# Optimization experiments

Measured on AMD Instinct MI355X. Metric: run time of the kernel, lower is better.

Reference implementation:

```python
import jax, jax.numpy as jnp
import numpy as np

B, S, C, H, D = 4, 2048, 512, 8, 64
EPS = 1e-5
SCALE = D ** -0.5


def layer_norm(x, w, b):
    m = jnp.mean(x, axis=-1, keepdims=True)
    v = jnp.var(x, axis=-1, keepdims=True)
    return (x - m) * jax.lax.rsqrt(v + EPS) * w + b


def setup_inputs() -> dict:
    key = jax.random.key(0)
    ks = jax.random.split(key, 7)
    s = 0.02
    return {
        "x": jax.random.normal(ks[0], (B, S, C), jnp.float32),
        "Wq": jax.random.normal(ks[1], (C, H * D), jnp.float32) * s,
        "Wk": jax.random.normal(ks[2], (C, H * D), jnp.float32) * s,
        "Wv": jax.random.normal(ks[3], (C, H * D), jnp.float32) * s,
        "Wo": jax.random.normal(ks[4], (H * D, C), jnp.float32) * s,
        "ln1_w": jnp.ones((C,), jnp.float32), "ln1_b": jnp.zeros((C,), jnp.float32),
        "ff_ln1_w": jnp.ones((C,), jnp.float32), "ff_ln1_b": jnp.zeros((C,), jnp.float32),
        "ff_w1": jax.random.normal(ks[5], (C, C), jnp.float32) * s, "ff_b1": jnp.zeros((C,), jnp.float32),
        "ff_ln2_w": jnp.ones((C,), jnp.float32), "ff_ln2_b": jnp.zeros((C,), jnp.float32),
        "ff_w2": jax.random.normal(ks[6], (C, C), jnp.float32) * s, "ff_b2": jnp.zeros((C,), jnp.float32),
        "ln2_w": jnp.ones((C,), jnp.float32), "ln2_b": jnp.zeros((C,), jnp.float32),
    }


def causal_attention(x, Wq, Wk, Wv, Wo):
    # Mathematically identical to the bucketed memory-efficient attention:
    # online-softmax bucketing changes compute order, not the result.
    q = (x @ Wq).reshape(B, S, H, D).transpose(0, 2, 1, 3)  # [B,H,S,D]
    k = (x @ Wk).reshape(B, S, H, D).transpose(0, 2, 1, 3)
    v = (x @ Wv).reshape(B, S, H, D).transpose(0, 2, 1, 3)
    scores = jnp.einsum('bhqd,bhkd->bhqk', q, k) * SCALE  # [B,H,S,S]
    causal = jnp.tril(jnp.ones((S, S), bool))
    scores = jnp.where(causal, scores, jnp.finfo(scores.dtype).min)
    attn = jax.nn.softmax(scores, axis=-1)
    out = jnp.einsum('bhqk,bhkd->bhqd', attn, v)
    out = out.transpose(0, 2, 1, 3).reshape(B, S, H * D)
    return out @ Wo


def reference(x, Wq, Wk, Wv, Wo, ln1_w, ln1_b, ff_ln1_w, ff_ln1_b, ff_w1, ff_b1,
              ff_ln2_w, ff_ln2_b, ff_w2, ff_b2, ln2_w, ln2_b):
    a = causal_attention(x, Wq, Wk, Wv, Wo)
    x_ln = layer_norm(a + x, ln1_w, ln1_b)
    h = layer_norm(x_ln, ff_ln1_w, ff_ln1_b) @ ff_w1 + ff_b1
    h = layer_norm(h, ff_ln2_w, ff_ln2_b) @ ff_w2 + ff_b2
    return layer_norm(h + x_ln, ln2_w, ln2_b)
```

## Files before the change

kernel.cpp:

```cpp
#include <hip/hip_runtime.h>

#define B_ 4
#define S_ 2048
#define C_ 512
#define H_ 8
#define D_ 64
#define M_ 8192

typedef short s8v __attribute__((ext_vector_type(8)));
typedef short s4v __attribute__((ext_vector_type(4)));
typedef float f4v __attribute__((ext_vector_type(4)));
typedef unsigned short u16;
typedef unsigned int u32;

__device__ __forceinline__ u16 f2b(float f) {
    u32 u = __builtin_bit_cast(u32, f);
    u = u + 0x7fffu + ((u >> 16) & 1u);
    return (u16)(u >> 16);
}

__device__ __forceinline__ void b2f8(const s8v v, float* f) {
    #pragma unroll
    for (int k = 0; k < 8; ++k)
        f[k] = __builtin_bit_cast(float, (u32)(u16)v[k] << 16);
}

__device__ __forceinline__ void gl2lds16(const void* g, void* l) {
    __builtin_amdgcn_global_load_lds(
        (const __attribute__((address_space(1))) void*)g,
        (__attribute__((address_space(3))) void*)l, 16, 0, 0);
}

__global__ __launch_bounds__(256) void prep_k(const float* __restrict__ x,
                                              u16* __restrict__ xb,
                                              const float* __restrict__ s0,
                                              const float* __restrict__ s1,
                                              const float* __restrict__ s2,
                                              const float* __restrict__ s3,
                                              const float* __restrict__ s4,
                                              const float* __restrict__ s5,
                                              u16* __restrict__ d0,
                                              u16* __restrict__ d1,
                                              u16* __restrict__ d2,
                                              u16* __restrict__ d3,
                                              u16* __restrict__ d4,
                                              u16* __restrict__ d5)
{
    __shared__ float t[32][33];
    const int bx = blockIdx.x;
    if (bx < 4096) {
        const int i = (bx * 256 + (int)threadIdx.x) * 4;
        const float4 v = *(const float4*)&x[i];
        ushort4 o;
        o.x = f2b(v.x); o.y = f2b(v.y); o.z = f2b(v.z); o.w = f2b(v.w);
        *(ushort4*)&xb[i] = o;
        return;
    }
    const int tb = bx - 4096;
    const int z = tb >> 8, rem = tb & 255;
    const float* W; u16* Wt;
    switch (z) {
        case 0: W = s0; Wt = d0; break;
        case 1: W = s1; Wt = d1; break;
        case 2: W = s2; Wt = d2; break;
        case 3: W = s3; Wt = d3; break;
        case 4: W = s4; Wt = d4; break;
        default: W = s5; Wt = d5; break;
    }
    const int tx = threadIdx.x & 31, ty = threadIdx.x >> 5;
    const int n0 = (rem & 15) * 32, k0 = (rem >> 4) * 32;
    #pragma unroll
    for (int i = 0; i < 4; ++i)
        t[ty + i * 8][tx] = W[(size_t)(k0 + ty + i * 8) * C_ + n0 + tx];
    __syncthreads();
    #pragma unroll
    for (int i = 0; i < 4; ++i)
        Wt[(size_t)(n0 + ty + i * 8) * C_ + k0 + tx] = f2b(t[tx][ty + i * 8]);
}

template <bool OB>
__global__ __launch_bounds__(256) void gemm_k(const u16* __restrict__ A,
                                              const u16* __restrict__ Bt,
                                              const float* __restrict__ bias,
                                              void* __restrict__ outv)
{
    __shared__ u16 As[2][128][64];
    __shared__ u16 Bs[2][64][64];
    const int tid = threadIdx.x;
    const int lane = tid & 63, w = tid >> 6;
    const int q4 = lane >> 4, l16 = lane & 15;
    const int wr = w >> 1, wc = w & 1;
    const int bm = blockIdx.x * 128, bn = blockIdx.y * 64;
    const int sr8  = lane >> 3;
    const int scol = ((lane & 7) ^ sr8) * 8;

    f4v acc[4][2];
    #pragma unroll
    for (int i = 0; i < 4; ++i)
        #pragma unroll
        for (int j = 0; j < 2; ++j) acc[i][j] = (f4v){0.f, 0.f, 0.f, 0.f};

    const u16* Ab = A  + (size_t)bm * C_;
    const u16* Bb = Bt + (size_t)bn * C_;

    auto stage = [&](int bf, int kt) {
        const int k0 = kt * 64;
        #pragma unroll
        for (int t = 0; t < 4; ++t)
            gl2lds16(Ab + (size_t)(w * 32 + t * 8 + sr8) * C_ + k0 + scol,
                     (char*)As + bf * 16384 + (w * 32 + t * 8) * 128);
        #pragma unroll
        for (int t = 0; t < 2; ++t)
            gl2lds16(Bb + (size_t)(w * 16 + t * 8 + sr8) * C_ + k0 + scol,
                     (char*)Bs + bf * 8192 + (w * 16 + t * 8) * 128);
    };

    stage(0, 0);
    for (int kt = 0; kt < 8; ++kt) {
        __syncthreads();
        const int bf = kt & 1;
        if (kt < 7) stage(bf ^ 1, kt + 1);
        #pragma unroll
        for (int kk = 0; kk < 2; ++kk) {
            const int pc = ((kk * 4 + q4) ^ (l16 & 7)) * 8;
            s8v a[4], b[2];
            #pragma unroll
            for (int i = 0; i < 4; ++i)
                a[i] = *(const s8v*)&As[bf][wr * 64 + i * 16 + l16][pc];
            #pragma unroll
            for (int j = 0; j < 2; ++j)
                b[j] = *(const s8v*)&Bs[bf][wc * 32 + j * 16 + l16][pc];
            #pragma unroll
            for (int i = 0; i < 4; ++i)
                #pragma unroll
                for (int j = 0; j < 2; ++j)
                    acc[i][j] = __builtin_amdgcn_mfma_f32_16x16x32_bf16(a[i], b[j], acc[i][j], 0, 0, 0);
        }
    }

    #pragma unroll
    for (int j = 0; j < 2; ++j) {
        const int n = bn + wc * 32 + j * 16 + l16;
        const float bj = bias ? bias[n] : 0.0f;
        #pragma unroll
        for (int i = 0; i < 4; ++i) {
            const int m = bm + wr * 64 + i * 16 + q4 * 4;
            #pragma unroll
            for (int reg = 0; reg < 4; ++reg) {
                const float vv = acc[i][j][reg] + bj;
                if constexpr (OB) ((u16*)outv)[(size_t)(m + reg) * C_ + n] = f2b(vv);
                else              ((float*)outv)[(size_t)(m + reg) * C_ + n] = vv;
            }
        }
    }
}

__global__ __launch_bounds__(256) void qkv_k(const u16* __restrict__ A,
                                             const u16* __restrict__ Wq,
                                             const u16* __restrict__ Wk,
                                             const u16* __restrict__ Wv,
                                             u16* __restrict__ oq,
                                             u16* __restrict__ ok,
                                             u16* __restrict__ ovt)
{
    __shared__ u16 As[2][128][64];
    __shared__ u16 Bs[2][64][64];
    const int tid = threadIdx.x;
    const int lane = tid & 63, w = tid >> 6;
    const int q4 = lane >> 4, l16 = lane & 15;
    const int wr = w >> 1, wc = w & 1;
    const int nt = blockIdx.y, which = nt >> 3;
    const u16* Bt = which == 0 ? Wq : (which == 1 ? Wk : Wv);
    const int bm = blockIdx.x * 128, bn = (nt & 7) * 64;
    const int sr8  = lane >> 3;
    const int scol = ((lane & 7) ^ sr8) * 8;

    f4v acc[4][2];
    #pragma unroll
    for (int i = 0; i < 4; ++i)
        #pragma unroll
        for (int j = 0; j < 2; ++j) acc[i][j] = (f4v){0.f, 0.f, 0.f, 0.f};

    const u16* Ab = A  + (size_t)bm * C_;
    const u16* Bb = Bt + (size_t)bn * C_;

    auto stage = [&](int bf, int kt) {
        const int k0 = kt * 64;
        #pragma unroll
        for (int t = 0; t < 4; ++t)
            gl2lds16(Ab + (size_t)(w * 32 + t * 8 + sr8) * C_ + k0 + scol,
                     (char*)As + bf * 16384 + (w * 32 + t * 8) * 128);
        #pragma unroll
        for (int t = 0; t < 2; ++t)
            gl2lds16(Bb + (size_t)(w * 16 + t * 8 + sr8) * C_ + k0 + scol,
                     (char*)Bs + bf * 8192 + (w * 16 + t * 8) * 128);
    };

    stage(0, 0);
    for (int kt = 0; kt < 8; ++kt) {
        __syncthreads();
        const int bf = kt & 1;
        if (kt < 7) stage(bf ^ 1, kt + 1);
        #pragma unroll
        for (int kk = 0; kk < 2; ++kk) {
            const int pc = ((kk * 4 + q4) ^ (l16 & 7)) * 8;
            s8v a[4], b[2];
            #pragma unroll
            for (int i = 0; i < 4; ++i)
                a[i] = *(const s8v*)&As[bf][wr * 64 + i * 16 + l16][pc];
            #pragma unroll
            for (int j = 0; j < 2; ++j)
                b[j] = *(const s8v*)&Bs[bf][wc * 32 + j * 16 + l16][pc];
            #pragma unroll
            for (int i = 0; i < 4; ++i)
                #pragma unroll
                for (int j = 0; j < 2; ++j)
                    acc[i][j] = __builtin_amdgcn_mfma_f32_16x16x32_bf16(a[i], b[j], acc[i][j], 0, 0, 0);
        }
    }

    if (which == 0) {
        #pragma unroll
        for (int j = 0; j < 2; ++j) {
            const int n = bn + wc * 32 + j * 16 + l16;
            #pragma unroll
            for (int i = 0; i < 4; ++i) {
                const int m = bm + wr * 64 + i * 16 + q4 * 4;
                #pragma unroll
                for (int reg = 0; reg < 4; ++reg)
                    oq[(size_t)(m + reg) * C_ + n] = f2b(acc[i][j][reg]);
            }
        }
    } else if (which == 1) {
        #pragma unroll
        for (int j = 0; j < 2; ++j) {
            const int n = bn + wc * 32 + j * 16 + l16;
            const int nswz = (n & ~31) | ((((n >> 3) & 3) ^ q4) << 3) | (n & 7);
            #pragma unroll
            for (int i = 0; i < 4; ++i) {
                const int m = bm + wr * 64 + i * 16 + q4 * 4;
                #pragma unroll
                for (int reg = 0; reg < 4; ++reg)
                    ok[(size_t)(m + reg) * C_ + nswz] = f2b(acc[i][j][reg]);
            }
        }
    } else {
        const int bglob = bm >> 11;
        const int sbase = bm & (S_ - 1);
        #pragma unroll
        for (int j = 0; j < 2; ++j) {
            const int n = bn + wc * 32 + j * 16 + l16;
            const int h = n >> 6, d = n & 63;
            u16* vrow = ovt + ((size_t)(bglob * H_ + h) * D_ + d) * S_;
            const int xw = d & 7;
            #pragma unroll
            for (int i = 0; i < 4; ++i) {
                const int s = sbase + wr * 64 + i * 16 + q4 * 4;
                const int pg = ((s & 31) >> 2) ^ xw;
                s4v pv;
                #pragma unroll
                for (int reg = 0; reg < 4; ++reg) pv[reg] = (short)f2b(acc[i][j][reg]);
                *(s4v*)&vrow[(s & ~31) + (pg << 2)] = pv;
            }
        }
    }
}

__global__ __launch_bounds__(256) void ln2xb_k(const u16* __restrict__ in,
                                               const float* __restrict__ res,
                                               const float* __restrict__ w1,
                                               const float* __restrict__ b1,
                                               const float* __restrict__ w2,
                                               const float* __restrict__ b2,
                                               u16* __restrict__ out1,
                                               u16* __restrict__ out2)
{
    const int lane = threadIdx.x & 63;
    const int row  = blockIdx.x * 4 + (threadIdx.x >> 6);
    const size_t off = (size_t)row * C_ + lane * 8;
    float v[8];
    b2f8(*(const s8v*)&in[off], v);
    {
        const float4 r0 = *(const float4*)&res[off];
        const float4 r1 = *(const float4*)&res[off + 4];
        v[0] += r0.x; v[1] += r0.y; v[2] += r0.z; v[3] += r0.w;
        v[4] += r1.x; v[5] += r1.y; v[6] += r1.z; v[7] += r1.w;
    }
    float s = 0.f, ss = 0.f;
    #pragma unroll
    for (int k = 0; k < 8; ++k) { s += v[k]; ss += v[k] * v[k]; }
    #pragma unroll
    for (int o = 32; o >= 1; o >>= 1) { s += __shfl_xor(s, o); ss += __shfl_xor(ss, o); }
    float mean = s * (1.0f / C_);
    float rstd = rsqrtf(ss * (1.0f / C_) - mean * mean + 1e-5f);

    const float4 wA0 = *(const float4*)&w1[lane * 8];
    const float4 wA1 = *(const float4*)&w1[lane * 8 + 4];
    const float4 bA0 = *(const float4*)&b1[lane * 8];
    const float4 bA1 = *(const float4*)&b1[lane * 8 + 4];
    const float wA[8] = {wA0.x, wA0.y, wA0.z, wA0.w, wA1.x, wA1.y, wA1.z, wA1.w};
    const float bA[8] = {bA0.x, bA0.y, bA0.z, bA0.w, bA1.x, bA1.y, bA1.z, bA1.w};
    float y[8];
    s8v o1;
    #pragma unroll
    for (int k = 0; k < 8; ++k) {
        y[k] = (v[k] - mean) * rstd * wA[k] + bA[k];
        o1[k] = (short)f2b(y[k]);
    }
    *(s8v*)&out1[off] = o1;

    s = 0.f; ss = 0.f;
    #pragma unroll
    for (int k = 0; k < 8; ++k) { s += y[k]; ss += y[k] * y[k]; }
    #pragma unroll
    for (int o = 32; o >= 1; o >>= 1) { s += __shfl_xor(s, o); ss += __shfl_xor(ss, o); }
    mean = s * (1.0f / C_);
    rstd = rsqrtf(ss * (1.0f / C_) - mean * mean + 1e-5f);

    const float4 wB0 = *(const float4*)&w2[lane * 8];
    const float4 wB1 = *(const float4*)&w2[lane * 8 + 4];
    const float4 bB0 = *(const float4*)&b2[lane * 8];
    const float4 bB1 = *(const float4*)&b2[lane * 8 + 4];
    const float wB[8] = {wB0.x, wB0.y, wB0.z, wB0.w, wB1.x, wB1.y, wB1.z, wB1.w};
    const float bB[8] = {bB0.x, bB0.y, bB0.z, bB0.w, bB1.x, bB1.y, bB1.z, bB1.w};
    s8v o2;
    #pragma unroll
    for (int k = 0; k < 8; ++k)
        o2[k] = (short)f2b((y[k] - mean) * rstd * wB[k] + bB[k]);
    *(s8v*)&out2[off] = o2;
}

__global__ __launch_bounds__(256) void lnb_k(const u16* __restrict__ in,
                                             const float* __restrict__ w,
                                             const float* __restrict__ bb,
                                             u16* __restrict__ out)
{
    const int lane = threadIdx.x & 63;
    const int row  = blockIdx.x * 4 + (threadIdx.x >> 6);
    const size_t off = (size_t)row * C_ + lane * 8;
    float v[8];
    b2f8(*(const s8v*)&in[off], v);
    float s = 0.f, ss = 0.f;
    #pragma unroll
    for (int k = 0; k < 8; ++k) { s += v[k]; ss += v[k] * v[k]; }
    #pragma unroll
    for (int o = 32; o >= 1; o >>= 1) { s += __shfl_xor(s, o); ss += __shfl_xor(ss, o); }
    const float mean = s * (1.0f / C_);
    const float rstd = rsqrtf(ss * (1.0f / C_) - mean * mean + 1e-5f);
    const float4 w0 = *(const float4*)&w[lane * 8];
    const float4 w1 = *(const float4*)&w[lane * 8 + 4];
    const float4 b0 = *(const float4*)&bb[lane * 8];
    const float4 b1 = *(const float4*)&bb[lane * 8 + 4];
    const float wv[8] = {w0.x, w0.y, w0.z, w0.w, w1.x, w1.y, w1.z, w1.w};
    const float bv[8] = {b0.x, b0.y, b0.z, b0.w, b1.x, b1.y, b1.z, b1.w};
    s8v o;
    #pragma unroll
    for (int k = 0; k < 8; ++k)
        o[k] = (short)f2b((v[k] - mean) * rstd * wv[k] + bv[k]);
    *(s8v*)&out[off] = o;
}

__global__ __launch_bounds__(256) void lnfin_k(const u16* __restrict__ in,
                                               const u16* __restrict__ res,
                                               const float* __restrict__ w,
                                               const float* __restrict__ bb,
                                               float* __restrict__ out)
{
    const int lane = threadIdx.x & 63;
    const int row  = blockIdx.x * 4 + (threadIdx.x >> 6);
    const size_t off = (size_t)row * C_ + lane * 8;
    float v[8], r[8];
    b2f8(*(const s8v*)&in[off], v);
    b2f8(*(const s8v*)&res[off], r);
    #pragma unroll
    for (int k = 0; k < 8; ++k) v[k] += r[k];
    float s = 0.f, ss = 0.f;
    #pragma unroll
    for (int k = 0; k < 8; ++k) { s += v[k]; ss += v[k] * v[k]; }
    #pragma unroll
    for (int o = 32; o >= 1; o >>= 1) { s += __shfl_xor(s, o); ss += __shfl_xor(ss, o); }
    const float mean = s * (1.0f / C_);
    const float rstd = rsqrtf(ss * (1.0f / C_) - mean * mean + 1e-5f);
    const float4 w0 = *(const float4*)&w[lane * 8];
    const float4 w1 = *(const float4*)&w[lane * 8 + 4];
    const float4 b0 = *(const float4*)&bb[lane * 8];
    const float4 b1 = *(const float4*)&bb[lane * 8 + 4];
    const float wv[8] = {w0.x, w0.y, w0.z, w0.w, w1.x, w1.y, w1.z, w1.w};
    const float bv[8] = {b0.x, b0.y, b0.z, b0.w, b1.x, b1.y, b1.z, b1.w};
    float4 o0, o1;
    o0.x = (v[0] - mean) * rstd * wv[0] + bv[0];
    o0.y = (v[1] - mean) * rstd * wv[1] + bv[1];
    o0.z = (v[2] - mean) * rstd * wv[2] + bv[2];
    o0.w = (v[3] - mean) * rstd * wv[3] + bv[3];
    o1.x = (v[4] - mean) * rstd * wv[4] + bv[4];
    o1.y = (v[5] - mean) * rstd * wv[5] + bv[5];
    o1.z = (v[6] - mean) * rstd * wv[6] + bv[6];
    o1.w = (v[7] - mean) * rstd * wv[7] + bv[7];
    *(float4*)&out[off]     = o0;
    *(float4*)&out[off + 4] = o1;
}

__global__ __launch_bounds__(256) void attn_k(const u16* __restrict__ Q,
                                              const u16* __restrict__ K,
                                              const u16* __restrict__ Vt,
                                              u16* __restrict__ O)
{
    __shared__ u16 Ks[2][2][64][32];
    __shared__ u16 Vs[2][2][64][32];
    const int tid = threadIdx.x;
    const int lane = tid & 63, w = tid >> 6;
    const int q4 = lane >> 4, l16 = lane & 15;
    const int h = blockIdx.y, b = blockIdx.z;
    const int qb = 31 - (int)blockIdx.x;
    const size_t base  = ((size_t)b * S_) * C_ + h * D_;
    const size_t basev = ((size_t)(b * H_ + h)) * D_ * S_;
    const int lr = lane >> 2, lc = (lane & 3) * 8;
    const int kq = (q4 ^ ((l16 >> 2) & 3)) * 8;

    s8v qf[2];
    #pragma unroll
    for (int kh = 0; kh < 2; ++kh)
        qf[kh] = *(const s8v*)&Q[base + (size_t)(qb * 64 + w * 16 + l16) * C_ + kh * 32 + q4 * 8];

    #pragma unroll
    for (int r = 0; r < 2; ++r) {
        const int seg = r * 4 + w;
        const int row = (seg & 3) * 16 + lr;
        const int kh = seg >> 2;
        gl2lds16(K  + base  + (size_t)row * C_ + kh * 32 + lc, (char*)Ks + seg * 1024);
        gl2lds16(Vt + basev + (size_t)row * S_ + kh * 32 + lc, (char*)Vs + seg * 1024);
    }

    f4v o[4];
    float lp[4] = {0.f, 0.f, 0.f, 0.f};
    #pragma unroll
    for (int j = 0; j < 4; ++j) o[j] = (f4v){0.f, 0.f, 0.f, 0.f};

    const int qrow = w * 16 + l16;
    for (int kb = 0; kb <= qb; ++kb) {
        __syncthreads();
        const int buf = kb & 1;
        if (kb < qb) {
            const int nb = buf ^ 1, kn = kb + 1;
            #pragma unroll
            for (int r = 0; r < 2; ++r) {
                const int seg = r * 4 + w;
                const int row = (seg & 3) * 16 + lr;
                const int kh = seg >> 2;
                gl2lds16(K  + base  + (size_t)(kn * 64 + row) * C_ + kh * 32 + lc,
                         (char*)Ks + nb * 8192 + seg * 1024);
                gl2lds16(Vt + basev + (size_t)row * S_ + kn * 64 + kh * 32 + lc,
                         (char*)Vs + nb * 8192 + seg * 1024);
            }
        }

        f4v sc[4];
        #pragma unroll
        for (int j = 0; j < 4; ++j) sc[j] = (f4v){0.f, 0.f, 0.f, 0.f};
        #pragma unroll
        for (int kh = 0; kh < 2; ++kh) {
            #pragma unroll
            for (int j = 0; j < 4; ++j) {
                const s8v kf = *(const s8v*)&Ks[buf][kh][j * 16 + l16][kq];
                sc[j] = __builtin_amdgcn_mfma_f32_16x16x32_bf16(kf, qf[kh], sc[j], 0, 0, 0);
            }
        }

        s4v pa[4];
        if (kb == qb) {
            #pragma unroll
            for (int j = 0; j < 4; ++j) {
                float ps = 0.0f;
                #pragma unroll
                for (int reg = 0; reg < 4; ++reg) {
                    float t = fmaf(sc[j][reg], 0.18033688011112043f, -11.541560327111707f);
                    if ((j * 16 + q4 * 4 + reg) > qrow) t = -128.0f;
                    const float p = exp2f(t);
                    ps += p;
                    pa[j][reg] = (short)(__builtin_bit_cast(u32, p) >> 16);
                }
                lp[j] += ps;
            }
        } else {
            #pragma unroll
            for (int j = 0; j < 4; ++j) {
                float ps = 0.0f;
                #pragma unroll
                for (int reg = 0; reg < 4; ++reg) {
                    const float p = exp2f(fmaf(sc[j][reg], 0.18033688011112043f,
                                               -11.541560327111707f));
                    ps += p;
                    pa[j][reg] = (short)(__builtin_bit_cast(u32, p) >> 16);
                }
                lp[j] += ps;
            }
        }

        #pragma unroll
        for (int c = 0; c < 4; ++c) {
            const int gh = (((c & 1) * 4 + q4) ^ (l16 & 7)) * 4;
            #pragma unroll
            for (int dj = 0; dj < 4; ++dj) {
                const s4v vb = *(const s4v*)&Vs[buf][c >> 1][dj * 16 + l16][gh];
                o[dj] = __builtin_amdgcn_mfma_f32_16x16x16bf16_1k(pa[c], vb, o[dj], 0, 0, 0);
            }
        }
    }

    float lt = (lp[0] + lp[1]) + (lp[2] + lp[3]);
    lt += __shfl_xor(lt, 16);
    lt += __shfl_xor(lt, 32);
    #pragma unroll
    for (int reg = 0; reg < 4; ++reg) {
        const float inv = 1.0f / __shfl(lt, q4 * 4 + reg);
        const size_t rowoff = base + (size_t)(qb * 64 + w * 16 + q4 * 4 + reg) * C_;
        #pragma unroll
        for (int dj = 0; dj < 4; ++dj)
            O[rowoff + dj * 16 + l16] = f2b(o[dj][reg] * inv);
    }
}

extern "C" void kernel_launch(void* const* d_in, const int* in_sizes, int n_in,
                              void* d_out, int out_size, void* d_ws, size_t ws_size,
                              hipStream_t stream)
{
    const float* x       = (const float*)d_in[0];
    const float* Wq      = (const float*)d_in[1];
    const float* Wk      = (const float*)d_in[2];
    const float* Wv      = (const float*)d_in[3];
    const float* Wo      = (const float*)d_in[4];
    const float* ln1_w   = (const float*)d_in[5];
    const float* ln1_b   = (const float*)d_in[6];
    const float* ffln1_w = (const float*)d_in[7];
    const float* ffln1_b = (const float*)d_in[8];
    const float* ff_w1   = (const float*)d_in[9];
    const float* ff_b1   = (const float*)d_in[10];
    const float* ffln2_w = (const float*)d_in[11];
    const float* ffln2_b = (const float*)d_in[12];
    const float* ff_w2   = (const float*)d_in[13];
    const float* ff_b2   = (const float*)d_in[14];
    const float* ln2_w   = (const float*)d_in[15];
    const float* ln2_b   = (const float*)d_in[16];
    float* out = (float*)d_out;

    const size_t MC = (size_t)M_ * C_;
    const size_t WW = (size_t)C_ * C_;
    u16* xb   = (u16*)d_ws;
    u16* WqT  = xb + MC;
    u16* WkT  = WqT + WW;
    u16* WvT  = WkT + WW;
    u16* WoT  = WvT + WW;
    u16* W1T  = WoT + WW;
    u16* W2T  = W1T + WW;
    u16* qbuf = W2T + WW;
    u16* kbuf = qbuf + MC;
    u16* vbuf = kbuf + MC;
    u16* vtbuf= vbuf + MC;
    u16*  abuf = xb;
    u16*  tf   = qbuf;
    u16*  xln  = vbuf;

    const dim3 gg(M_ / 128, C_ / 64);
    const dim3 gq(M_ / 128, 24);
    const dim3 ga(32, H_, B_);
    const int  gl = M_ / 4;

    prep_k<<<5632, 256, 0, stream>>>(x, xb, Wq, Wk, Wv, Wo, ff_w1, ff_w2,
                                     WqT, WkT, WvT, WoT, W1T, W2T);

    qkv_k<<<gq, 256, 0, stream>>>(xb, WqT, WkT, WvT, qbuf, kbuf, vtbuf);
    attn_k<<<ga, 256, 0, stream>>>(qbuf, kbuf, vtbuf, abuf);

    gemm_k<true><<<gg, 256, 0, stream>>>(abuf, WoT, nullptr, tf);
    ln2xb_k<<<gl, 256, 0, stream>>>(tf, x, ln1_w, ln1_b, ffln1_w, ffln1_b,
                                    xln, xb);
    gemm_k<true><<<gg, 256, 0, stream>>>(xb, W1T, ff_b1, tf);
    lnb_k<<<gl, 256, 0, stream>>>(tf, ffln2_w, ffln2_b, xb);
    gemm_k<true><<<gg, 256, 0, stream>>>(xb, W2T, ff_b2, tf);
    lnfin_k<<<gl, 256, 0, stream>>>(tf, xln, ln2_w, ln2_b, out);
}
```

Baseline: 242.7 us.

## Pair causal query blocks per workgroup and raise MFMA wave priority

Each attention workgroup now handles two query blocks, qb and 31-qb, so every workgroup does the same amount of causal work. The grid halves to 16 blocks in x. The first K/V tile for the second block is prefetched while the first block's output is written. s_setprio is raised around the MFMA sections so matrix work gets issue priority over other waves. The cost is half as many workgroups (512), which lowers parallelism and occupancy slack. Each workgroup also runs sequentially for longer.

```diff
diff --git a/kernel.cpp b/kernel.cpp
--- a/kernel.cpp
+++ b/kernel.cpp
@@ -411,113 +411,136 @@
     const int lane = tid & 63, w = tid >> 6;
     const int q4 = lane >> 4, l16 = lane & 15;
     const int h = blockIdx.y, b = blockIdx.z;
-    const int qb = 31 - (int)blockIdx.x;
     const size_t base  = ((size_t)b * S_) * C_ + h * D_;
     const size_t basev = ((size_t)(b * H_ + h)) * D_ * S_;
     const int lr = lane >> 2, lc = (lane & 3) * 8;
     const int kq = (q4 ^ ((l16 >> 2) & 3)) * 8;
-
+    const int qrow = w * 16 + l16;
+
+    const u16* kbase = K  + base  + (size_t)(w * 16 + lr) * C_ + lc;
+    const u16* vbase = Vt + basev + (size_t)(w * 16 + lr) * S_ + lc;
+    char* kd0 = (char*)Ks + w * 1024;
+    char* kd1 = (char*)Ks + (4 + w) * 1024;
+    char* vd0 = (char*)Vs + w * 1024;
+    char* vd1 = (char*)Vs + (4 + w) * 1024;
+
+    f4v o[4];
+    float lp[4];
     s8v qf[2];
-    #pragma unroll
-    for (int kh = 0; kh < 2; ++kh)
-        qf[kh] = *(const s8v*)&Q[base + (size_t)(qb * 64 + w * 16 + l16) * C_ + kh * 32 + q4 * 8];
-
-    #pragma unroll
-    for (int r = 0; r < 2; ++r) {
-        const int seg = r * 4 + w;
-        const int row = (seg & 3) * 16 + lr;
-        const int kh = seg >> 2;
-        gl2lds16(K  + base  + (size_t)row * C_ + kh * 32 + lc, (char*)Ks + seg * 1024);
-        gl2lds16(Vt + basev + (size_t)row * S_ + kh * 32 + lc, (char*)Vs + seg * 1024);
-    }
-
-    f4v o[4];
-    float lp[4] = {0.f, 0.f, 0.f, 0.f};
-    #pragma unroll
-    for (int j = 0; j < 4; ++j) o[j] = (f4v){0.f, 0.f, 0.f, 0.f};
-
-    const int qrow = w * 16 + l16;
-    for (int kb = 0; kb <= qb; ++kb) {
-        __syncthreads();
-        const int buf = kb & 1;
-        if (kb < qb) {
-            const int nb = buf ^ 1, kn = kb + 1;
-            #pragma unroll
-            for (int r = 0; r < 2; ++r) {
-                const int seg = r * 4 + w;
-                const int row = (seg & 3) * 16 + lr;
-                const int kh = seg >> 2;
-                gl2lds16(K  + base  + (size_t)(kn * 64 + row) * C_ + kh * 32 + lc,
-                         (char*)Ks + nb * 8192 + seg * 1024);
-                gl2lds16(Vt + basev + (size_t)row * S_ + kn * 64 + kh * 32 + lc,
-                         (char*)Vs + nb * 8192 + seg * 1024);
-            }
-        }
-
-        f4v sc[4];
-        #pragma unroll
-        for (int j = 0; j < 4; ++j) sc[j] = (f4v){0.f, 0.f, 0.f, 0.f};
-        #pragma unroll
-        for (int kh = 0; kh < 2; ++kh) {
-            #pragma unroll
-            for (int j = 0; j < 4; ++j) {
-                const s8v kf = *(const s8v*)&Ks[buf][kh][j * 16 + l16][kq];
-                sc[j] = __builtin_amdgcn_mfma_f32_16x16x32_bf16(kf, qf[kh], sc[j], 0, 0, 0);
-            }
-        }
-
-        s4v pa[4];
-        if (kb == qb) {
-            #pragma unroll
-            for (int j = 0; j < 4; ++j) {
-                float ps = 0.0f;
-                #pragma unroll
-                for (int reg = 0; reg < 4; ++reg) {
-                    float t = fmaf(sc[j][reg], 0.18033688011112043f, -11.541560327111707f);
-                    if ((j * 16 + q4 * 4 + reg) > qrow) t = -128.0f;
-                    const float p = exp2f(t);
-                    ps += p;
-                    pa[j][reg] = (short)(__builtin_bit_cast(u32, p) >> 16);
+
+    auto stage0 = [&]() {
+        gl2lds16(kbase,      kd0);
+        gl2lds16(kbase + 32, kd1);
+        gl2lds16(vbase,      vd0);
+        gl2lds16(vbase + 32, vd1);
+    };
+    auto loadq = [&](int qb) {
+        #pragma unroll
+        for (int kh = 0; kh < 2; ++kh)
+            qf[kh] = *(const s8v*)&Q[base + (size_t)(qb * 64 + qrow) * C_ + kh * 32 + q4 * 8];
+        #pragma unroll
+        for (int j = 0; j < 4; ++j) { o[j] = (f4v){0.f, 0.f, 0.f, 0.f}; lp[j] = 0.f; }
+    };
+
+    auto kbloop = [&](int qb) {
+        const u16* kp = kbase + 64 * C_;
+        const u16* vp = vbase + 64;
+        for (int kb = 0; kb <= qb; ++kb) {
+            __syncthreads();
+            const int buf = kb & 1;
+            if (kb < qb) {
+                const int nb = (buf ^ 1) * 8192;
+                gl2lds16(kp,      kd0 + nb);
+                gl2lds16(kp + 32, kd1 + nb);
+                gl2lds16(vp,      vd0 + nb);
+                gl2lds16(vp + 32, vd1 + nb);
+                kp += 64 * C_;
+                vp += 64;
+            }
+
+            f4v sc[4];
+            #pragma unroll
+            for (int j = 0; j < 4; ++j) sc[j] = (f4v){0.f, 0.f, 0.f, 0.f};
+            __builtin_amdgcn_s_setprio(1);
+            #pragma unroll
+            for (int kh = 0; kh < 2; ++kh) {
+                #pragma unroll
+                for (int j = 0; j < 4; ++j) {
+                    const s8v kf = *(const s8v*)&Ks[buf][kh][j * 16 + l16][kq];
+                    sc[j] = __builtin_amdgcn_mfma_f32_16x16x32_bf16(kf, qf[kh], sc[j], 0, 0, 0);
                 }
-                lp[j] += ps;
-            }
-        } else {
-            #pragma unroll
-            for (int j = 0; j < 4; ++j) {
-                float ps = 0.0f;
-                #pragma unroll
-                for (int reg = 0; reg < 4; ++reg) {
-                    const float p = exp2f(fmaf(sc[j][reg], 0.18033688011112043f,
-                                               -11.541560327111707f));
-                    ps += p;
-                    pa[j][reg] = (short)(__builtin_bit_cast(u32, p) >> 16);
+            }
+            __builtin_amdgcn_s_setprio(0);
+
+            s4v pa[4];
+            if (kb == qb) {
+                #pragma unroll
+                for (int j = 0; j < 4; ++j) {
+                    float ps = 0.0f;
+                    #pragma unroll
+                    for (int reg = 0; reg < 4; ++reg) {
+                        float t = fmaf(sc[j][reg], 0.18033688011112043f, -11.541560327111707f);
+                        if ((j * 16 + q4 * 4 + reg) > qrow) t = -128.0f;
+                        const float p = exp2f(t);
+                        ps += p;
+                        pa[j][reg] = (short)(__builtin_bit_cast(u32, p) >> 16);
+                    }
+                    lp[j] += ps;
                 }
-                lp[j] += ps;
-            }
-        }
-
-        #pragma unroll
-        for (int c = 0; c < 4; ++c) {
-            const int gh = (((c & 1) * 4 + q4) ^ (l16 & 7)) * 4;
-            #pragma unroll
-            for (int dj = 0; dj < 4; ++dj) {
-                const s4v vb = *(const s4v*)&Vs[buf][c >> 1][dj * 16 + l16][gh];
-                o[dj] = __builtin_amdgcn_mfma_f32_16x16x16bf16_1k(pa[c], vb, o[dj], 0, 0, 0);
-            }
-        }
-    }
-
-    float lt = (lp[0] + lp[1]) + (lp[2] + lp[3]);
-    lt += __shfl_xor(lt, 16);
-    lt += __shfl_xor(lt, 32);
-    #pragma unroll
-    for (int reg = 0; reg < 4; ++reg) {
-        const float inv = 1.0f / __shfl(lt, q4 * 4 + reg);
-        const size_t rowoff = base + (size_t)(qb * 64 + w * 16 + q4 * 4 + reg) * C_;
-        #pragma unroll
-        for (int dj = 0; dj < 4; ++dj)
-            O[rowoff + dj * 16 + l16] = f2b(o[dj][reg] * inv);
-    }
+            } else {
+                #pragma unroll
+                for (int j = 0; j < 4; ++j) {
+                    float ps = 0.0f;
+                    #pragma unroll
+                    for (int reg = 0; reg < 4; ++reg) {
+                        const float p = exp2f(fmaf(sc[j][reg], 0.18033688011112043f,
+                                                   -11.541560327111707f));
+                        ps += p;
+                        pa[j][reg] = (short)(__builtin_bit_cast(u32, p) >> 16);
+                    }
+                    lp[j] += ps;
+                }
+            }
+
+            __builtin_amdgcn_s_setprio(1);
+            #pragma unroll
+            for (int c = 0; c < 4; ++c) {
+                const int gh = (((c & 1) * 4 + q4) ^ (l16 & 7)) * 4;
+                #pragma unroll
+                for (int dj = 0; dj < 4; ++dj) {
+                    const s4v vb = *(const s4v*)&Vs[buf][c >> 1][dj * 16 + l16][gh];
+                    o[dj] = __builtin_amdgcn_mfma_f32_16x16x16bf16_1k(pa[c], vb, o[dj], 0, 0, 0);
+                }
+            }
+            __builtin_amdgcn_s_setprio(0);
+        }
+    };
+
+    auto writeout = [&](int qb) {
+        float lt = (lp[0] + lp[1]) + (lp[2] + lp[3]);
+        lt += __shfl_xor(lt, 16);
+        lt += __shfl_xor(lt, 32);
+        #pragma unroll
+        for (int reg = 0; reg < 4; ++reg) {
+            const float inv = 1.0f / __shfl(lt, q4 * 4 + reg);
+            const size_t rowoff = base + (size_t)(qb * 64 + w * 16 + q4 * 4 + reg) * C_;
+            #pragma unroll
+            for (int dj = 0; dj < 4; ++dj)
+                O[rowoff + dj * 16 + l16] = f2b(o[dj][reg] * inv);
+        }
+    };
+
+    int qb = 31 - (int)blockIdx.x;
+    stage0();
+    loadq(qb);
+    kbloop(qb);
+    __syncthreads();
+    stage0();
+    writeout(qb);
+    const int qb1 = (int)blockIdx.x;
+    loadq(qb1);
+    kbloop(qb1);
+    writeout(qb1);
 }
 
 extern "C" void kernel_launch(void* const* d_in, const int* in_sizes, int n_in,
@@ -562,7 +585,7 @@
 
     const dim3 gg(M_ / 128, C_ / 64);
     const dim3 gq(M_ / 128, 24);
-    const dim3 ga(32, H_, B_);
+    const dim3 ga(16, H_, B_);
     const int  gl = M_ / 4;
 
     prep_k<<<5632, 256, 0, stream>>>(x, xb, Wq, Wk, Wv, Wo, ff_w1, ff_w2,
```

Measured after the change: 228.5 us. -5.9%, faster.

## Pair causal query blocks per workgroup and split KV steps across two wave groups

Applied to the files above, without the earlier changes.

The attention kernel now processes a heavy and a light query block (qH=31-px, qL=px) in one 512-thread workgroup, so every block does exactly 33 KV tiles and the causal work is balanced. Two groups of four waves take alternating KV steps through a 4-slot LDS ring, then merge their partial accumulators and row sums through shared memory before normalising. It also raises MFMA sections with s_setprio. The grid is halved, and LDS use grows to 64KB per block, which may limit occupancy and adds a reduction step.

```diff
diff --git a/kernel.cpp b/kernel.cpp
--- a/kernel.cpp
+++ b/kernel.cpp
@@ -400,123 +400,209 @@
     *(float4*)&out[off + 4] = o1;
 }
 
-__global__ __launch_bounds__(256) void attn_k(const u16* __restrict__ Q,
-                                              const u16* __restrict__ K,
-                                              const u16* __restrict__ Vt,
-                                              u16* __restrict__ O)
-{
-    __shared__ u16 Ks[2][2][64][32];
-    __shared__ u16 Vs[2][2][64][32];
+__global__ __launch_bounds__(512, 4) void attn_k(const u16* __restrict__ Q,
+                                                 const u16* __restrict__ K,
+                                                 const u16* __restrict__ Vt,
+                                                 u16* __restrict__ O)
+{
+    __shared__ char smem[65536];
+    u16* KsB = (u16*)smem;
+    u16* VsB = (u16*)(smem + 32768);
     const int tid = threadIdx.x;
     const int lane = tid & 63, w = tid >> 6;
+    const int grp = w >> 2, wl = w & 3;
     const int q4 = lane >> 4, l16 = lane & 15;
     const int h = blockIdx.y, b = blockIdx.z;
-    const int qb = 31 - (int)blockIdx.x;
+    const int px = blockIdx.x;
+    const int qH = 31 - px, qL = px;
+    const int nH = 32 - px;
     const size_t base  = ((size_t)b * S_) * C_ + h * D_;
     const size_t basev = ((size_t)(b * H_ + h)) * D_ * S_;
     const int lr = lane >> 2, lc = (lane & 3) * 8;
     const int kq = (q4 ^ ((l16 >> 2) & 3)) * 8;
+    const int qrow = wl * 16 + l16;
+
+    auto stage = [&](int kb, int sl) {
+        #pragma unroll
+        for (int r = 0; r < 2; ++r) {
+            const int seg = r * 4 + wl;
+            const int row = (seg & 3) * 16 + lr;
+            const int kh = seg >> 2;
+            gl2lds16(K  + base  + (size_t)(kb * 64 + row) * C_ + kh * 32 + lc,
+                     (char*)KsB + sl * 8192 + seg * 1024);
+            gl2lds16(Vt + basev + (size_t)row * S_ + kb * 64 + kh * 32 + lc,
+                     (char*)VsB + sl * 8192 + seg * 1024);
+        }
+    };
 
     s8v qf[2];
     #pragma unroll
     for (int kh = 0; kh < 2; ++kh)
-        qf[kh] = *(const s8v*)&Q[base + (size_t)(qb * 64 + w * 16 + l16) * C_ + kh * 32 + q4 * 8];
-
-    #pragma unroll
-    for (int r = 0; r < 2; ++r) {
-        const int seg = r * 4 + w;
-        const int row = (seg & 3) * 16 + lr;
-        const int kh = seg >> 2;
-        gl2lds16(K  + base  + (size_t)row * C_ + kh * 32 + lc, (char*)Ks + seg * 1024);
-        gl2lds16(Vt + basev + (size_t)row * S_ + kh * 32 + lc, (char*)Vs + seg * 1024);
-    }
-
-    f4v o[4];
-    float lp[4] = {0.f, 0.f, 0.f, 0.f};
-    #pragma unroll
-    for (int j = 0; j < 4; ++j) o[j] = (f4v){0.f, 0.f, 0.f, 0.f};
-
-    const int qrow = w * 16 + l16;
-    for (int kb = 0; kb <= qb; ++kb) {
+        qf[kh] = *(const s8v*)&Q[base + (size_t)(qH * 64 + qrow) * C_ + kh * 32 + q4 * 8];
+
+    f4v acc[4]; float lp[4];
+    f4v oH[4];  float lpH[4];
+    #pragma unroll
+    for (int j = 0; j < 4; ++j) {
+        acc[j] = (f4v){0.f, 0.f, 0.f, 0.f}; lp[j] = 0.f;
+        oH[j]  = (f4v){0.f, 0.f, 0.f, 0.f}; lpH[j] = 0.f;
+    }
+    bool dumped = false;
+
+    stage(grp, grp);
+
+    for (int t = 0; t <= 16; ++t) {
         __syncthreads();
-        const int buf = kb & 1;
-        if (kb < qb) {
-            const int nb = buf ^ 1, kn = kb + 1;
-            #pragma unroll
-            for (int r = 0; r < 2; ++r) {
-                const int seg = r * 4 + w;
-                const int row = (seg & 3) * 16 + lr;
-                const int kh = seg >> 2;
-                gl2lds16(K  + base  + (size_t)(kn * 64 + row) * C_ + kh * 32 + lc,
-                         (char*)Ks + nb * 8192 + seg * 1024);
-                gl2lds16(Vt + basev + (size_t)row * S_ + kn * 64 + kh * 32 + lc,
-                         (char*)Vs + nb * 8192 + seg * 1024);
-            }
-        }
-
-        f4v sc[4];
-        #pragma unroll
-        for (int j = 0; j < 4; ++j) sc[j] = (f4v){0.f, 0.f, 0.f, 0.f};
-        #pragma unroll
-        for (int kh = 0; kh < 2; ++kh) {
-            #pragma unroll
-            for (int j = 0; j < 4; ++j) {
-                const s8v kf = *(const s8v*)&Ks[buf][kh][j * 16 + l16][kq];
-                sc[j] = __builtin_amdgcn_mfma_f32_16x16x32_bf16(kf, qf[kh], sc[j], 0, 0, 0);
-            }
-        }
-
-        s4v pa[4];
-        if (kb == qb) {
-            #pragma unroll
-            for (int j = 0; j < 4; ++j) {
-                float ps = 0.0f;
-                #pragma unroll
-                for (int reg = 0; reg < 4; ++reg) {
-                    float t = fmaf(sc[j][reg], 0.18033688011112043f, -11.541560327111707f);
-                    if ((j * 16 + q4 * 4 + reg) > qrow) t = -128.0f;
-                    const float p = exp2f(t);
-                    ps += p;
-                    pa[j][reg] = (short)(__builtin_bit_cast(u32, p) >> 16);
+        const int s = 2 * t + grp;
+        if (s <= 32) {
+            const int s2 = s + 2;
+            if (s2 <= 32) {
+                const int kb2 = s2 < nH ? s2 : s2 - nH;
+                stage(kb2, s2 & 3);
+            }
+            if (s >= nH && !dumped) {
+                dumped = true;
+                #pragma unroll
+                for (int j = 0; j < 4; ++j) {
+                    oH[j] = acc[j]; lpH[j] = lp[j];
+                    acc[j] = (f4v){0.f, 0.f, 0.f, 0.f}; lp[j] = 0.f;
                 }
-                lp[j] += ps;
-            }
+                #pragma unroll
+                for (int kh = 0; kh < 2; ++kh)
+                    qf[kh] = *(const s8v*)&Q[base + (size_t)(qL * 64 + qrow) * C_ + kh * 32 + q4 * 8];
+            }
+            const int kb = s < nH ? s : s - nH;
+            const int sl = s & 3;
+            const u16* ks = KsB + sl * 4096;
+            const u16* vs = VsB + sl * 4096;
+
+            f4v sc[4];
+            #pragma unroll
+            for (int j = 0; j < 4; ++j) sc[j] = (f4v){0.f, 0.f, 0.f, 0.f};
+            __builtin_amdgcn_s_setprio(1);
+            #pragma unroll
+            for (int kh = 0; kh < 2; ++kh) {
+                #pragma unroll
+                for (int j = 0; j < 4; ++j) {
+                    const s8v kf = *(const s8v*)&ks[(kh * 64 + j * 16 + l16) * 32 + kq];
+                    sc[j] = __builtin_amdgcn_mfma_f32_16x16x32_bf16(kf, qf[kh], sc[j], 0, 0, 0);
+                }
+            }
+            __builtin_amdgcn_s_setprio(0);
+
+            s4v pa[4];
+            const bool diag = (s == nH - 1) || (s == 32);
+            if (diag) {
+                #pragma unroll
+                for (int j = 0; j < 4; ++j) {
+                    float ps = 0.0f;
+                    #pragma unroll
+                    for (int reg = 0; reg < 4; ++reg) {
+                        float tt = fmaf(sc[j][reg], 0.18033688011112043f, -11.541560327111707f);
+                        if ((j * 16 + q4 * 4 + reg) > qrow) tt = -128.0f;
+                        const float p = exp2f(tt);
+                        ps += p;
+                        pa[j][reg] = (short)(__builtin_bit_cast(u32, p) >> 16);
+                    }
+                    lp[j] += ps;
+                }
+            } else {
+                #pragma unroll
+                for (int j = 0; j < 4; ++j) {
+                    float ps = 0.0f;
+                    #pragma unroll
+                    for (int reg = 0; reg < 4; ++reg) {
+                        const float p = exp2f(fmaf(sc[j][reg], 0.18033688011112043f,
+                                                   -11.541560327111707f));
+                        ps += p;
+                        pa[j][reg] = (short)(__builtin_bit_cast(u32, p) >> 16);
+                    }
+                    lp[j] += ps;
+                }
+            }
+
+            __builtin_amdgcn_s_setprio(1);
+            #pragma unroll
+            for (int c = 0; c < 4; ++c) {
+                const int gh = (((c & 1) * 4 + q4) ^ (l16 & 7)) * 4;
+                #pragma unroll
+                for (int dj = 0; dj < 4; ++dj) {
+                    const s4v vb = *(const s4v*)&vs[((c >> 1) * 64 + dj * 16 + l16) * 32 + gh];
+                    acc[dj] = __builtin_amdgcn_mfma_f32_16x16x16bf16_1k(pa[c], vb, acc[dj], 0, 0, 0);
+                }
+            }
+            __builtin_amdgcn_s_setprio(0);
+        }
+    }
+
+    if (!dumped) {
+        #pragma unroll
+        for (int j = 0; j < 4; ++j) {
+            oH[j] = acc[j]; lpH[j] = lp[j];
+            acc[j] = (f4v){0.f, 0.f, 0.f, 0.f}; lp[j] = 0.f;
+        }
+    }
+
+    __syncthreads();
+    float* exH = (float*)smem;
+    float* exL = (float*)(smem + 20480);
+    {
+        float* p = (grp ? exH : exL) + (wl * 64 + lane) * 20;
+        if (grp) {
+            #pragma unroll
+            for (int dj = 0; dj < 4; ++dj)
+                #pragma unroll
+                for (int reg = 0; reg < 4; ++reg) p[dj * 4 + reg] = oH[dj][reg];
+            #pragma unroll
+            for (int j = 0; j < 4; ++j) p[16 + j] = lpH[j];
         } else {
             #pragma unroll
-            for (int j = 0; j < 4; ++j) {
-                float ps = 0.0f;
-                #pragma unroll
-                for (int reg = 0; reg < 4; ++reg) {
-                    const float p = exp2f(fmaf(sc[j][reg], 0.18033688011112043f,
-                                               -11.541560327111707f));
-                    ps += p;
-                    pa[j][reg] = (short)(__builtin_bit_cast(u32, p) >> 16);
-                }
-                lp[j] += ps;
-            }
-        }
-
-        #pragma unroll
-        for (int c = 0; c < 4; ++c) {
-            const int gh = (((c & 1) * 4 + q4) ^ (l16 & 7)) * 4;
-            #pragma unroll
-            for (int dj = 0; dj < 4; ++dj) {
-                const s4v vb = *(const s4v*)&Vs[buf][c >> 1][dj * 16 + l16][gh];
-                o[dj] = __builtin_amdgcn_mfma_f32_16x16x16bf16_1k(pa[c], vb, o[dj], 0, 0, 0);
-            }
-        }
-    }
-
-    float lt = (lp[0] + lp[1]) + (lp[2] + lp[3]);
-    lt += __shfl_xor(lt, 16);
-    lt += __shfl_xor(lt, 32);
-    #pragma unroll
-    for (int reg = 0; reg < 4; ++reg) {
-        const float inv = 1.0f / __shfl(lt, q4 * 4 + reg);
-        const size_t rowoff = base + (size_t)(qb * 64 + w * 16 + q4 * 4 + reg) * C_;
+            for (int dj = 0; dj < 4; ++dj)
+                #pragma unroll
+                for (int reg = 0; reg < 4; ++reg) p[dj * 4 + reg] = acc[dj][reg];
+            #pragma unroll
+            for (int j = 0; j < 4; ++j) p[16 + j] = lp[j];
+        }
+    }
+    __syncthreads();
+    if (grp == 0) {
+        const float* p = exH + (wl * 64 + lane) * 20;
         #pragma unroll
         for (int dj = 0; dj < 4; ++dj)
-            O[rowoff + dj * 16 + l16] = f2b(o[dj][reg] * inv);
+            #pragma unroll
+            for (int reg = 0; reg < 4; ++reg) oH[dj][reg] += p[dj * 4 + reg];
+        #pragma unroll
+        for (int j = 0; j < 4; ++j) lpH[j] += p[16 + j];
+        float lt = (lpH[0] + lpH[1]) + (lpH[2] + lpH[3]);
+        lt += __shfl_xor(lt, 16);
+        lt += __shfl_xor(lt, 32);
+        #pragma unroll
+        for (int reg = 0; reg < 4; ++reg) {
+            const float inv = 1.0f / __shfl(lt, q4 * 4 + reg);
+            const size_t rowoff = base + (size_t)(qH * 64 + wl * 16 + q4 * 4 + reg) * C_;
+            #pragma unroll
+            for (int dj = 0; dj < 4; ++dj)
+                O[rowoff + dj * 16 + l16] = f2b(oH[dj][reg] * inv);
+        }
+    } else {
+        const float* p = exL + (wl * 64 + lane) * 20;
+        #pragma unroll
+        for (int dj = 0; dj < 4; ++dj)
+            #pragma unroll
+            for (int reg = 0; reg < 4; ++reg) acc[dj][reg] += p[dj * 4 + reg];
+        #pragma unroll
+        for (int j = 0; j < 4; ++j) lp[j] += p[16 + j];
+        float lt = (lp[0] + lp[1]) + (lp[2] + lp[3]);
+        lt += __shfl_xor(lt, 16);
+        lt += __shfl_xor(lt, 32);
+        #pragma unroll
+        for (int reg = 0; reg < 4; ++reg) {
+            const float inv = 1.0f / __shfl(lt, q4 * 4 + reg);
+            const size_t rowoff = base + (size_t)(qL * 64 + wl * 16 + q4 * 4 + reg) * C_;
+            #pragma unroll
+            for (int dj = 0; dj < 4; ++dj)
+                O[rowoff + dj * 16 + l16] = f2b(acc[dj][reg] * inv);
+        }
     }
 }
 
@@ -562,14 +648,14 @@
 
     const dim3 gg(M_ / 128, C_ / 64);
     const dim3 gq(M_ / 128, 24);
-    const dim3 ga(32, H_, B_);
+    const dim3 ga(16, H_, B_);
     const int  gl = M_ / 4;
 
     prep_k<<<5632, 256, 0, stream>>>(x, xb, Wq, Wk, Wv, Wo, ff_w1, ff_w2,
                                      WqT, WkT, WvT, WoT, W1T, W2T);
 
     qkv_k<<<gq, 256, 0, stream>>>(xb, WqT, WkT, WvT, qbuf, kbuf, vtbuf);
-    attn_k<<<ga, 256, 0, stream>>>(qbuf, kbuf, vtbuf, abuf);
+    attn_k<<<ga, 512, 0, stream>>>(qbuf, kbuf, vtbuf, abuf);
 
     gemm_k<true><<<gg, 256, 0, stream>>>(abuf, WoT, nullptr, tf);
     ln2xb_k<<<gl, 256, 0, stream>>>(tf, x, ln1_w, ln1_b, ffln1_w, ffln1_b,
```

Result: faster. 230.5 us (-5.0%).
